# Kernel tuning notes

Hardware: AMD Instinct MI355X
Metric: run time of the kernel (lower is better)

Reference implementation:

```python
import jax, jax.numpy as jnp
import numpy as np

TOP_K = 2

def setup_inputs() -> dict:
    key = jax.random.key(0)
    k1, k2 = jax.random.split(key)
    x = jax.random.normal(k1, (8, 4096, 4096), dtype=jnp.float32)
    # nn.Linear weight [num_experts, dim]
    gate_w = jax.random.normal(k2, (64, 4096), dtype=jnp.float32) * (1.0 / np.sqrt(4096))
    return {"x": x, "gate_w": gate_w}

def reference(x, gate_w):
    # logits: [B, S, E]
    logits = jnp.einsum('bsd,ed->bse', x, gate_w)
    routing_weights = jax.nn.softmax(logits, axis=-1)
    top_weights, top_indices = jax.lax.top_k(routing_weights, TOP_K)
    top_weights = top_weights / jnp.sum(top_weights, axis=-1, keepdims=True)
    return top_weights, top_indices
```

## Files before the change

kernel.cpp:

```cpp
#include <hip/hip_runtime.h>
#include <hip/hip_bf16.h>
#include <math.h>


typedef __attribute__((ext_vector_type(8))) short short8;
typedef __attribute__((ext_vector_type(4))) float f32x4;

#define TAU 1e-4f
#define LROW 68

__device__ __forceinline__ void cvt8(const f32x4* v, short8* hi, short8* lo) {
    const float* f = reinterpret_cast<const float*>(v);
#pragma unroll
    for (int j = 0; j < 8; ++j) {
        __hip_bfloat16 h = __float2bfloat16(f[j]);
        float r = f[j] - __bfloat162float(h);
        __hip_bfloat16 l = __float2bfloat16(r);
        (*hi)[j] = (short)*reinterpret_cast<unsigned short*>(&h);
        (*lo)[j] = (short)*reinterpret_cast<unsigned short*>(&l);
    }
}

__global__ void prep_b(const float* __restrict__ gw,
                       short8* __restrict__ bh, short8* __restrict__ bl) {
    const int tid = blockIdx.x * 256 + threadIdx.x;
    const int ln  = tid & 63;
    const int w   = (tid >> 6) & 127;
    const int nt  = tid >> 13;
    const int row = nt * 16 + (ln & 15);
    const int k   = w * 32 + ((ln >> 4) << 3);
    f32x4 v[2];
    v[0] = *reinterpret_cast<const f32x4*>(gw + (long)row * 4096 + k);
    v[1] = *reinterpret_cast<const f32x4*>(gw + (long)row * 4096 + k + 4);
    short8 h, l;
    cvt8(v, &h, &l);
    bh[tid] = h;
    bl[tid] = l;
}

__device__ __forceinline__ void gload16(const void* g, void* l) {
    __builtin_amdgcn_global_load_lds(
        (const __attribute__((address_space(1))) void*)g,
        (__attribute__((address_space(3))) void*)l, 16, 0, 0);
}

#define STAGE(C, BUF) do {                                                    \
    char* aB = &AB[(BUF) * 16384];                                            \
    char* bB = &AB[32768 + (BUF) * 16384];                                    \
    _Pragma("unroll")                                                         \
    for (int i = 0; i < 4; ++i)                                               \
        gload16(srcA[i] + (C) * 256, aB + (wv * 16 + i * 4) * 256);           \
    _Pragma("unroll")                                                         \
    for (int i = 0; i < 4; ++i) {                                             \
        const int seg = wv * 4 + i;                                           \
        const short8* sp = ((seg & 1) ? blp : bhp)                            \
            + (((seg >> 1) & 3) * 8192 + (2 * (C) + (seg >> 3)) * 64 + ln);   \
        gload16(sp, bB + seg * 1024);                                         \
    }                                                                         \
} while (0)

#define COMPUTE(BUF) do {                                                     \
    const char* aB = &AB[(BUF) * 16384];                                      \
    const char* bB = &AB[32768 + (BUF) * 16384];                              \
    _Pragma("unroll")                                                         \
    for (int w = 0; w < 2; ++w) {                                             \
        f32x4 av[2];                                                          \
        const int rbase = (wv * 16 + fr) * 256;                               \
        av[0] = *(const f32x4*)(aB + rbase + (((w * 8 + q * 2 + 0) ^ fr) * 16)); \
        av[1] = *(const f32x4*)(aB + rbase + (((w * 8 + q * 2 + 1) ^ fr) * 16)); \
        short8 ah, al;                                                        \
        cvt8(av, &ah, &al);                                                   \
        _Pragma("unroll")                                                     \
        for (int nt = 0; nt < 4; ++nt) {                                      \
            short8 bh = *(const short8*)(bB + ((w * 4 + nt) * 2 + 0) * 1024 + ln * 16); \
            short8 bl = *(const short8*)(bB + ((w * 4 + nt) * 2 + 1) * 1024 + ln * 16); \
            acc[nt] = __builtin_amdgcn_mfma_f32_16x16x32_bf16(ah, bh, acc[nt], 0, 0, 0); \
            acc[nt] = __builtin_amdgcn_mfma_f32_16x16x32_bf16(ah, bl, acc[nt], 0, 0, 0); \
            acc[nt] = __builtin_amdgcn_mfma_f32_16x16x32_bf16(al, bh, acc[nt], 0, 0, 0); \
            acc[nt] = __builtin_amdgcn_mfma_f32_16x16x32_bf16(al, bl, acc[nt], 0, 0, 0); \
        }                                                                     \
    }                                                                         \
} while (0)

__global__ __launch_bounds__(256, 2)
void router_fused(const float* __restrict__ x,
                  const short8* __restrict__ bhp,
                  const short8* __restrict__ blp,
                  const float* __restrict__ gw,
                  float* __restrict__ out,
                  int M, int K) {
    __shared__ __align__(16) char AB[65536];
    __shared__ int flags[64];
    __shared__ double Ld4[4][64];

    const int t  = threadIdx.x;
    const int wv = t >> 6;
    const int ln = t & 63;
    const int fr = ln & 15;
    const int q  = ln >> 4;
    const long tok0 = (long)blockIdx.x * 64;

    const char* srcA[4];
#pragma unroll
    for (int i = 0; i < 4; ++i) {
        const int row  = wv * 16 + i * 4 + q;
        const int slot = (ln & 15) ^ (i * 4 + q);
        srcA[i] = (const char*)x + ((tok0 + row) * (long)K) * 4 + slot * 16;
    }

    f32x4 acc[4];
#pragma unroll
    for (int nt = 0; nt < 4; ++nt) acc[nt] = (f32x4){0.f, 0.f, 0.f, 0.f};

    STAGE(0, 0);
    __syncthreads();
    STAGE(1, 1);

    for (int c = 0; c < 64; ++c) {
        const int buf = c & 1;
        COMPUTE(buf);
        __syncthreads();
        if (c + 2 < 64) STAGE(c + 2, buf);
    }

    float* Ls = (float*)AB;
#pragma unroll
    for (int nt = 0; nt < 4; ++nt)
#pragma unroll
        for (int r = 0; r < 4; ++r)
            Ls[(wv * 16 + q * 4 + r) * LROW + nt * 16 + fr] = acc[nt][r];
    __syncthreads();

    if (t < 64) {
        const float* row = Ls + (long)t * LROW;
        float m1 = -INFINITY, m2 = -INFINITY, m3 = -INFINITY;
        int i1 = 0, i2 = 0;
#pragma unroll 8
        for (int e = 0; e < 64; ++e) {
            const float v = row[e];
            if (v > m1)      { m3 = m2; m2 = m1; i2 = i1; m1 = v; i1 = e; }
            else if (v > m2) { m3 = m2; m2 = v; i2 = e; }
            else if (v > m3) { m3 = v; }
        }
        const float e2 = expf(m2 - m1);
        const float s  = 1.0f + e2;

        const long g = tok0 + t;
        out[2 * g + 0] = 1.0f / s;
        out[2 * g + 1] = e2 / s;
        float* oi = out + 2 * (long)M;
        oi[2 * g + 0] = (float)i1;
        oi[2 * g + 1] = (float)i2;

        flags[t] = ((m1 - m2) < TAU) | ((m2 - m3) < TAU);
    }
    __syncthreads();

    for (int tk = 0; tk < 64; ++tk) {
        if (flags[tk]) {
            const float* xr = x + (tok0 + tk) * (long)K + wv * 1024;
            const float* gr = gw + (long)ln * (long)K + wv * 1024;
            double s0 = 0.0, s1 = 0.0, s2 = 0.0, s3 = 0.0;
            for (int k = 0; k < 1024; k += 4) {
                const f32x4 a = *reinterpret_cast<const f32x4*>(xr + k);
                const f32x4 b = *reinterpret_cast<const f32x4*>(gr + k);
                s0 = fma((double)a.x, (double)b.x, s0);
                s1 = fma((double)a.y, (double)b.y, s1);
                s2 = fma((double)a.z, (double)b.z, s2);
                s3 = fma((double)a.w, (double)b.w, s3);
            }
            Ld4[wv][ln] = (s0 + s1) + (s2 + s3);
            __syncthreads();
            if (t == 0) {
                double m1 = -INFINITY, m2 = -INFINITY;
                int i1 = 0, i2 = 0;
                for (int e = 0; e < 64; ++e) {
                    const double v = Ld4[0][e] + Ld4[1][e] + Ld4[2][e] + Ld4[3][e];
                    if (v > m1)      { m2 = m1; i2 = i1; m1 = v; i1 = e; }
                    else if (v > m2) { m2 = v; i2 = e; }
                }
                const double e2 = exp(m2 - m1);
                const double s  = 1.0 + e2;
                const long g = tok0 + tk;
                out[2 * g + 0] = (float)(1.0 / s);
                out[2 * g + 1] = (float)(e2 / s);
                float* oi = out + 2 * (long)M;
                oi[2 * g + 0] = (float)i1;
                oi[2 * g + 1] = (float)i2;
            }
            __syncthreads();
        }
    }
}

extern "C" void kernel_launch(void* const* d_in, const int* in_sizes, int n_in,
                              void* d_out, int out_size, void* d_ws, size_t ws_size,
                              hipStream_t stream) {
    const float* x  = (const float*)d_in[0];
    const float* gw = (const float*)d_in[1];
    float* out = (float*)d_out;

    const int K = 4096;
    const int M = in_sizes[0] / K;
    const int nblocks = M / 64;

    short8* bh = (short8*)d_ws;
    short8* bl = bh + 32768;

    prep_b<<<128, 256, 0, stream>>>(gw, bh, bl);
    router_fused<<<nblocks, 256, 0, stream>>>(x, bh, bl, gw, out, M, K);
}
```

Baseline: 242.9 us.

## Shrink router GEMM tile to 32 tokens with split waves and finer pipelining

Each block now handles 32 tokens instead of 64. The four waves are split 2x2 across the token rows and expert columns, and K is staged in 128 smaller chunks with explicit vmcnt waits and raw barriers. LDS use drops from 64KB to 24KB and the launch bound rises to 4 blocks per SM, so occupancy should go up and the load queue should stay fuller. In exchange, each block re-reads the bf16 hi/lo expert-weight tiles for half as many tokens, which doubles weight traffic from L2, and there are more barriers per unit of work.

```diff
diff --git a/kernel.cpp b/kernel.cpp
--- a/kernel.cpp
+++ b/kernel.cpp
@@ -6,6 +6,8 @@
 typedef __attribute__((ext_vector_type(8))) short short8;
 typedef __attribute__((ext_vector_type(4))) float f32x4;
 
+#define TPB 32
+#define NCH 128
 #define TAU 1e-4f
 #define LROW 68
 
@@ -45,52 +47,22 @@
 }
 
 #define STAGE(C, BUF) do {                                                    \
-    char* aB = &AB[(BUF) * 16384];                                            \
-    char* bB = &AB[32768 + (BUF) * 16384];                                    \
-    _Pragma("unroll")                                                         \
-    for (int i = 0; i < 4; ++i)                                               \
-        gload16(srcA[i] + (C) * 256, aB + (wv * 16 + i * 4) * 256);           \
-    _Pragma("unroll")                                                         \
-    for (int i = 0; i < 4; ++i) {                                             \
-        const int seg = wv * 4 + i;                                           \
-        const short8* sp = ((seg & 1) ? blp : bhp)                            \
-            + (((seg >> 1) & 3) * 8192 + (2 * (C) + (seg >> 3)) * 64 + ln);   \
-        gload16(sp, bB + seg * 1024);                                         \
-    }                                                                         \
+    char* aB = AB + (BUF) * 4096;                                             \
+    char* bB = AB + 8192 + (BUF) * 8192;                                      \
+    gload16(srcA + (long)(C) * 128, aB + wv * 1024 + ln * 16);                \
+    gload16(bhp + (long)wv * 8192 + (C) * 64 + ln, bB + (wv * 2 + 0) * 1024 + ln * 16); \
+    gload16(blp + (long)wv * 8192 + (C) * 64 + ln, bB + (wv * 2 + 1) * 1024 + ln * 16); \
 } while (0)
 
-#define COMPUTE(BUF) do {                                                     \
-    const char* aB = &AB[(BUF) * 16384];                                      \
-    const char* bB = &AB[32768 + (BUF) * 16384];                              \
-    _Pragma("unroll")                                                         \
-    for (int w = 0; w < 2; ++w) {                                             \
-        f32x4 av[2];                                                          \
-        const int rbase = (wv * 16 + fr) * 256;                               \
-        av[0] = *(const f32x4*)(aB + rbase + (((w * 8 + q * 2 + 0) ^ fr) * 16)); \
-        av[1] = *(const f32x4*)(aB + rbase + (((w * 8 + q * 2 + 1) ^ fr) * 16)); \
-        short8 ah, al;                                                        \
-        cvt8(av, &ah, &al);                                                   \
-        _Pragma("unroll")                                                     \
-        for (int nt = 0; nt < 4; ++nt) {                                      \
-            short8 bh = *(const short8*)(bB + ((w * 4 + nt) * 2 + 0) * 1024 + ln * 16); \
-            short8 bl = *(const short8*)(bB + ((w * 4 + nt) * 2 + 1) * 1024 + ln * 16); \
-            acc[nt] = __builtin_amdgcn_mfma_f32_16x16x32_bf16(ah, bh, acc[nt], 0, 0, 0); \
-            acc[nt] = __builtin_amdgcn_mfma_f32_16x16x32_bf16(ah, bl, acc[nt], 0, 0, 0); \
-            acc[nt] = __builtin_amdgcn_mfma_f32_16x16x32_bf16(al, bh, acc[nt], 0, 0, 0); \
-            acc[nt] = __builtin_amdgcn_mfma_f32_16x16x32_bf16(al, bl, acc[nt], 0, 0, 0); \
-        }                                                                     \
-    }                                                                         \
-} while (0)
-
-__global__ __launch_bounds__(256, 2)
+__global__ __launch_bounds__(256, 4)
 void router_fused(const float* __restrict__ x,
                   const short8* __restrict__ bhp,
                   const short8* __restrict__ blp,
                   const float* __restrict__ gw,
                   float* __restrict__ out,
                   int M, int K) {
-    __shared__ __align__(16) char AB[65536];
-    __shared__ int flags[64];
+    __shared__ __align__(16) char AB[24576];
+    __shared__ int flags[TPB];
     __shared__ double Ld4[4][64];
 
     const int t  = threadIdx.x;
@@ -98,40 +70,68 @@
     const int ln = t & 63;
     const int fr = ln & 15;
     const int q  = ln >> 4;
-    const long tok0 = (long)blockIdx.x * 64;
-
-    const char* srcA[4];
-#pragma unroll
-    for (int i = 0; i < 4; ++i) {
-        const int row  = wv * 16 + i * 4 + q;
-        const int slot = (ln & 15) ^ (i * 4 + q);
-        srcA[i] = (const char*)x + ((tok0 + row) * (long)K) * 4 + slot * 16;
-    }
-
-    f32x4 acc[4];
-#pragma unroll
-    for (int nt = 0; nt < 4; ++nt) acc[nt] = (f32x4){0.f, 0.f, 0.f, 0.f};
+    const int mm = wv >> 1;
+    const int nn = wv & 1;
+    const long tok0 = (long)blockIdx.x * TPB;
+
+    const int arow = wv * 8 + (ln >> 3);
+    const int sw   = (ln & 7) ^ (ln >> 3);
+    const char* srcA = (const char*)(x + (tok0 + arow) * (long)K) + sw * 16;
+
+    f32x4 acc[2];
+    acc[0] = (f32x4){0.f, 0.f, 0.f, 0.f};
+    acc[1] = (f32x4){0.f, 0.f, 0.f, 0.f};
 
     STAGE(0, 0);
+    STAGE(1, 1);
+
+    for (int c = 0; c < NCH; ++c) {
+        const int buf = c & 1;
+        if (c + 1 < NCH) asm volatile("s_waitcnt vmcnt(3)" ::: "memory");
+        else             asm volatile("s_waitcnt vmcnt(0)" ::: "memory");
+        __builtin_amdgcn_s_barrier();
+        asm volatile("" ::: "memory");
+        __builtin_amdgcn_sched_barrier(0);
+
+        {
+            const char* aB = AB + buf * 4096;
+            const char* bB = AB + 8192 + buf * 8192;
+            const int r = mm * 16 + fr;
+            f32x4 av[2];
+            av[0] = *(const f32x4*)(aB + r * 128 + (((q * 2 + 0) ^ (fr & 7)) * 16));
+            av[1] = *(const f32x4*)(aB + r * 128 + (((q * 2 + 1) ^ (fr & 7)) * 16));
+            short8 ah, al;
+            cvt8(av, &ah, &al);
+#pragma unroll
+            for (int ntl = 0; ntl < 2; ++ntl) {
+                const int nt = 2 * nn + ntl;
+                short8 bhv = *(const short8*)(bB + (nt * 2 + 0) * 1024 + ln * 16);
+                short8 blv = *(const short8*)(bB + (nt * 2 + 1) * 1024 + ln * 16);
+                acc[ntl] = __builtin_amdgcn_mfma_f32_16x16x32_bf16(ah, bhv, acc[ntl], 0, 0, 0);
+                acc[ntl] = __builtin_amdgcn_mfma_f32_16x16x32_bf16(ah, blv, acc[ntl], 0, 0, 0);
+                acc[ntl] = __builtin_amdgcn_mfma_f32_16x16x32_bf16(al, bhv, acc[ntl], 0, 0, 0);
+                acc[ntl] = __builtin_amdgcn_mfma_f32_16x16x32_bf16(al, blv, acc[ntl], 0, 0, 0);
+            }
+        }
+
+        __builtin_amdgcn_sched_barrier(0);
+        asm volatile("" ::: "memory");
+        __builtin_amdgcn_s_barrier();
+        asm volatile("" ::: "memory");
+        if (c + 2 < NCH) STAGE(c + 2, buf);
+        __builtin_amdgcn_sched_barrier(0);
+    }
+
     __syncthreads();
-    STAGE(1, 1);
-
-    for (int c = 0; c < 64; ++c) {
-        const int buf = c & 1;
-        COMPUTE(buf);
-        __syncthreads();
-        if (c + 2 < 64) STAGE(c + 2, buf);
-    }
-
     float* Ls = (float*)AB;
 #pragma unroll
-    for (int nt = 0; nt < 4; ++nt)
+    for (int ntl = 0; ntl < 2; ++ntl)
 #pragma unroll
         for (int r = 0; r < 4; ++r)
-            Ls[(wv * 16 + q * 4 + r) * LROW + nt * 16 + fr] = acc[nt][r];
+            Ls[(mm * 16 + q * 4 + r) * LROW + (2 * nn + ntl) * 16 + fr] = acc[ntl][r];
     __syncthreads();
 
-    if (t < 64) {
+    if (t < TPB) {
         const float* row = Ls + (long)t * LROW;
         float m1 = -INFINITY, m2 = -INFINITY, m3 = -INFINITY;
         int i1 = 0, i2 = 0;
@@ -156,7 +156,7 @@
     }
     __syncthreads();
 
-    for (int tk = 0; tk < 64; ++tk) {
+    for (int tk = 0; tk < TPB; ++tk) {
         if (flags[tk]) {
             const float* xr = x + (tok0 + tk) * (long)K + wv * 1024;
             const float* gr = gw + (long)ln * (long)K + wv * 1024;
@@ -202,7 +202,7 @@
 
     const int K = 4096;
     const int M = in_sizes[0] / K;
-    const int nblocks = M / 64;
+    const int nblocks = M / TPB;
 
     short8* bh = (short8*)d_ws;
     short8* bl = bh + 32768;
```

After: 236.3 us. -2.7%, faster.
